# Optimization experiments

Hardware: AMD Instinct MI355X
Metric: run time of the kernel (lower is better)

Reference implementation:

```python
import jax, jax.numpy as jnp
import numpy as np

# conv_ada hyperparameters from init_kwargs: ka=1, alpha=0.25, kw=0.2
KA1 = 1.0          # activation scale for conv1 (ka)
KA2 = 1.25         # activation scale for conv2 (ka + alpha)
KW = 0.2           # weight clipping threshold used by the binary weight STE


def ste_sign(x, clip=1.0):
    """Binary sign with straight-through estimator (hardtanh-style clip).
    Forward value is sign(x); gradient is that of clip(x, -clip, clip)."""
    xc = jnp.clip(x, -clip, clip)
    return xc + jax.lax.stop_gradient(jnp.sign(x) - xc)


def conv_bin(x, w, ka, kw):
    """1-bit activation / 1-bit weight 3x3 conv (conv_ada).
    Activations -> ka * sign(x); weights -> per-out-channel mean(|w|) * sign(w)."""
    xq = ka * ste_sign(x)
    alpha_w = jnp.mean(jnp.abs(w), axis=(1, 2, 3), keepdims=True)  # [O,1,1,1]
    wq = alpha_w * ste_sign(w, kw)
    return jax.lax.conv_general_dilated(
        xq, wq, window_strides=(1, 1), padding='SAME',
        dimension_numbers=('NCHW', 'OIHW', 'NCHW'))


def prelu(x, slope):
    # per-channel PReLU, slope shape [C]
    return jnp.where(x >= 0, x, slope[None, :, None, None] * x)


def pixel_shuffle(x, r=2):
    b, c, h, w = x.shape
    co = c // (r * r)
    x = x.reshape(b, co, r, r, h, w)
    x = x.transpose(0, 1, 4, 2, 5, 3)  # b, co, h, r, w, r
    return x.reshape(b, co, h * r, w * r)


def setup_inputs() -> dict:
    key = jax.random.key(0)
    ks = jax.random.split(key, 11)
    B, C, H, W = 8, 64, 256, 256
    return {
        'x': jax.random.normal(ks[0], (B, C, H, W), jnp.float32),
        'w1': jax.random.normal(ks[1], (C, C, 3, 3), jnp.float32) * 0.1,
        'w2': jax.random.normal(ks[2], (2 * C, C, 3, 3), jnp.float32) * 0.1,
        'b_in': jax.random.normal(ks[3], (1, C, 1, 1), jnp.float32) * 0.01,
        'b1': jax.random.normal(ks[4], (1, C, 1, 1), jnp.float32) * 0.01,
        's1': jax.random.uniform(ks[5], (C,), jnp.float32) * 0.25,
        'b2': jax.random.normal(ks[6], (1, C, 1, 1), jnp.float32) * 0.01,
        'b2_': jax.random.normal(ks[7], (1, C, 1, 1), jnp.float32) * 0.01,
        'b3': jax.random.normal(ks[8], (1, 2 * C, 1, 1), jnp.float32) * 0.01,
        's2': jax.random.uniform(ks[9], (2 * C,), jnp.float32) * 0.25,
        'b4': jax.random.normal(ks[10], (1, 2 * C, 1, 1), jnp.float32) * 0.01,
    }


def reference(x, w1, w2, b_in, b1, s1, b2, b2_, b3, s2, b4):
    out = conv_bin(x + b_in, w1, KA1, KW)       # move1_ -> conv1
    xres = out + x                              # residual x = out + x
    # NOTE: in the original forward, move1 -> prelu1 -> move2 are computed on
    # `out` and then immediately overwritten by out = move2_(x); that branch
    # is dead code and does not affect the output (b1, s1, b2 get zero grads).
    out = conv_bin(xres + b2_, w2, KA2, KW)     # move2_ -> conv2
    out = out + jnp.concatenate([xres, xres], axis=1)  # shortcut = cat(x, x)
    out = prelu(out + b3, s2) + b4              # move3 -> prelu2 -> move4
    return pixel_shuffle(out, 2)                # [B, C/2, 2H, 2W]
```

## Files before the change

### kernel.cpp

```cpp
#include <hip/hip_runtime.h>
#include <hip/hip_bf16.h>

typedef unsigned long long u64;
typedef unsigned short ushort8 __attribute__((ext_vector_type(8)));

#define IMG_H 256
#define IMG_W 256
#define CIN   64
#define HW    (IMG_H * IMG_W)
#define NPIX  (8 * HW)

static __device__ __forceinline__ float bf16bits_to_f32(unsigned short h) {
    union { unsigned int u; float f; } c;
    c.u = ((unsigned int)h) << 16;
    return c.f;
}

__global__ void prep_kernel(const float* __restrict__ w1,
                            const float* __restrict__ w2,
                            u64* __restrict__ w1b, float* __restrict__ a1,
                            u64* __restrict__ w2b, float* __restrict__ a2) {
    int blk = blockIdx.x;
    int lane = threadIdx.x;
    const float* w;
    u64* wb;
    float* al;
    if (blk < 64) { w = w1 + (size_t)blk * 576;        wb = w1b + blk * 9;        al = a1 + blk; }
    else          { w = w2 + (size_t)(blk - 64) * 576; wb = w2b + (blk - 64) * 9; al = a2 + (blk - 64); }

    const float* wi = w + lane * 9;
    float s = 0.f;
    u64 bits[9];
#pragma unroll
    for (int t = 0; t < 9; ++t) {
        float v = wi[t];
        s += fabsf(v);
        bits[t] = __ballot(v > 0.f);
    }
#pragma unroll
    for (int m = 32; m >= 1; m >>= 1) s += __shfl_xor(s, m);
    if (lane == 0) {
        *al = s * (1.f / 576.f);
#pragma unroll
        for (int t = 0; t < 9; ++t) wb[t] = bits[t];
    }
}

__global__ __launch_bounds__(256)
void pack_kernel(const float* __restrict__ x,
                 const float* __restrict__ b_in,
                 u64* __restrict__ bits1) {
    int i = blockIdx.x * 256 + threadIdx.x;
    int n = i >> 16, p = i & 65535;
    const float* xp = x + (size_t)n * CIN * HW + p;
    u64 w = 0;
#pragma unroll
    for (int c = 0; c < 64; ++c)
        w |= (u64)((xp[(size_t)c * HW] + b_in[c]) > 0.f) << c;
    bits1[i] = w;
}

__global__ __launch_bounds__(256)
void conv1_kernel(const float* __restrict__ x,
                  const float* __restrict__ b2_,
                  const u64* __restrict__ bits1,
                  const u64* __restrict__ wbits,
                  const float* __restrict__ alpha1,
                  ushort8* __restrict__ xres,
                  u64* __restrict__ bits2) {
    int i = blockIdx.x * 256 + threadIdx.x;
    int n = i >> 16, p = i & 65535;
    int y = p >> 8, xc = p & 255;

    u64 xb[9];
    int invmask = 0, nv = 0;
#pragma unroll
    for (int t = 0; t < 9; ++t) {
        int dy = t / 3 - 1, dx = t % 3 - 1;
        bool v = ((unsigned)(y + dy) < (unsigned)IMG_H) &
                 ((unsigned)(xc + dx) < (unsigned)IMG_W);
        xb[t] = v ? bits1[i + dy * IMG_W + dx] : 0ull;
        invmask |= (v ? 0 : 1) << t;
        nv += v ? 1 : 0;
    }

    const float* xp = x + (size_t)n * CIN * HW + p;
    u64 w2 = 0;

#pragma unroll 1
    for (int g = 0; g < 8; ++g) {
        ushort8 pk;
#pragma unroll
        for (int j = 0; j < 8; ++j) {
            int o = g * 8 + j;
            const u64* wo = wbits + o * 9;
            int D = 0;
#pragma unroll
            for (int t = 0; t < 9; ++t) D += __popcll(xb[t] ^ wo[t]);
            int S = 64 * nv - 2 * D;
            if (invmask) {
                int Dc = 0;
#pragma unroll
                for (int t = 0; t < 9; ++t)
                    if ((invmask >> t) & 1) Dc += __popcll(wo[t]);
                S += 2 * Dc;
            }
            float r = alpha1[o] * (float)S + xp[(size_t)o * HW];
            __hip_bfloat16 hb = __float2bfloat16(r);
            pk[j] = *(unsigned short*)&hb;
            w2 |= (u64)((r + b2_[o]) > 0.f) << o;
        }
        xres[(size_t)(n * 8 + g) * HW + p] = pk;
    }
    bits2[i] = w2;
}

__global__ __launch_bounds__(256)
void conv2_kernel(const ushort8* __restrict__ xres,
                  const u64* __restrict__ bits2,
                  const u64* __restrict__ wbits,
                  const float* __restrict__ alpha2,
                  const float* __restrict__ b3,
                  const float* __restrict__ s2,
                  const float* __restrict__ b4,
                  float* __restrict__ out) {
    int i = blockIdx.x * 256 + threadIdx.x;
    int n = i >> 16, p = i & 65535;
    int y = p >> 8, xc = p & 255;

    u64 xb[9];
    int invmask = 0, nv = 0;
#pragma unroll
    for (int t = 0; t < 9; ++t) {
        int dy = t / 3 - 1, dx = t % 3 - 1;
        bool v = ((unsigned)(y + dy) < (unsigned)IMG_H) &
                 ((unsigned)(xc + dx) < (unsigned)IMG_W);
        xb[t] = v ? bits2[i + dy * IMG_W + dx] : 0ull;
        invmask |= (v ? 0 : 1) << t;
        nv += v ? 1 : 0;
    }

    float* ob = out + (size_t)n * 32 * 512 * 512;
    const int Y = 2 * y, X = 2 * xc;

#pragma unroll 1
    for (int g = 0; g < 8; ++g) {
        ushort8 xr = xres[(size_t)(n * 8 + g) * HW + p];
        float vlo[8], vhi[8];
#pragma unroll
        for (int j = 0; j < 8; ++j) {
            int o = g * 8 + j;
            float xrv = bf16bits_to_f32(xr[j]);
            {
                const u64* wo = wbits + o * 9;
                int D = 0;
#pragma unroll
                for (int t = 0; t < 9; ++t) D += __popcll(xb[t] ^ wo[t]);
                int S = 64 * nv - 2 * D;
                if (invmask) {
                    int Dc = 0;
#pragma unroll
                    for (int t = 0; t < 9; ++t)
                        if ((invmask >> t) & 1) Dc += __popcll(wo[t]);
                    S += 2 * Dc;
                }
                float u = 1.25f * alpha2[o] * (float)S + xrv + b3[o];
                u = (u >= 0.f) ? u : s2[o] * u;
                vlo[j] = u + b4[o];
            }
            {
                int o2 = o + 64;
                const u64* wo = wbits + o2 * 9;
                int D = 0;
#pragma unroll
                for (int t = 0; t < 9; ++t) D += __popcll(xb[t] ^ wo[t]);
                int S = 64 * nv - 2 * D;
                if (invmask) {
                    int Dc = 0;
#pragma unroll
                    for (int t = 0; t < 9; ++t)
                        if ((invmask >> t) & 1) Dc += __popcll(wo[t]);
                    S += 2 * Dc;
                }
                float u = 1.25f * alpha2[o2] * (float)S + xrv + b3[o2];
                u = (u >= 0.f) ? u : s2[o2] * u;
                vhi[j] = u + b4[o2];
            }
        }
#pragma unroll
        for (int jj = 0; jj < 8; jj += 2) {
            int o = g * 8 + jj;
            int co = o >> 2;
            int r1 = (o >> 1) & 1;
            *(float2*)(ob + ((size_t)co * 512 + Y + r1) * 512 + X) =
                make_float2(vlo[jj], vlo[jj + 1]);
            *(float2*)(ob + ((size_t)(co + 16) * 512 + Y + r1) * 512 + X) =
                make_float2(vhi[jj], vhi[jj + 1]);
        }
    }
}

extern "C" void kernel_launch(void* const* d_in, const int* in_sizes, int n_in,
                              void* d_out, int out_size, void* d_ws, size_t ws_size,
                              hipStream_t stream) {
    const float* x    = (const float*)d_in[0];
    const float* w1   = (const float*)d_in[1];
    const float* w2   = (const float*)d_in[2];
    const float* b_in = (const float*)d_in[3];
    const float* b2_  = (const float*)d_in[7];
    const float* b3   = (const float*)d_in[8];
    const float* s2   = (const float*)d_in[9];
    const float* b4   = (const float*)d_in[10];
    float* out = (float*)d_out;

    char* ws = (char*)d_ws;
    u64*   w1b   = (u64*)(ws + 0);
    u64*   w2b   = (u64*)(ws + 4608);
    float* a1    = (float*)(ws + 13824);
    float* a2    = (float*)(ws + 14080);
    u64*   bits1 = (u64*)(ws + 16384);
    u64*   bits2 = (u64*)(ws + 16384 + 4194304);
    ushort8* xres = (ushort8*)(ws + 16384 + 2 * 4194304);

    prep_kernel<<<192, 64, 0, stream>>>(w1, w2, w1b, a1, w2b, a2);

    const int nblk = NPIX / 256;
    pack_kernel <<<nblk, 256, 0, stream>>>(x, b_in, bits1);
    conv1_kernel<<<nblk, 256, 0, stream>>>(x, b2_, bits1, w1b, a1, xres, bits2);
    conv2_kernel<<<nblk, 256, 0, stream>>>(xres, bits2, w2b, a2, b3, s2, b4, out);
}
```

Measured before the change: 241.6 us.

## Vectorize pack loads, hoist conv1 residual loads, unroll loops, nontemporal output stores

The pack kernel now has each thread handle two pixels, using float2 loads and a 128-bit store of the packed bits, so it launches half as many blocks. conv1 loads the eight residual x values per group up front and builds the sign mask eight bits at a time. Both conv loops are unrolled by two, and conv2 writes its output with nontemporal stores to avoid polluting the cache. These changes aim to cut memory-instruction overhead and raise memory-level parallelism, at the cost of higher register pressure from unrolling.

```diff
diff --git a/kernel.cpp b/kernel.cpp
--- a/kernel.cpp
+++ b/kernel.cpp
@@ -2,7 +2,10 @@
 #include <hip/hip_bf16.h>
 
 typedef unsigned long long u64;
+typedef unsigned int u32;
 typedef unsigned short ushort8 __attribute__((ext_vector_type(8)));
+typedef u64 u64x2 __attribute__((ext_vector_type(2)));
+typedef float fx2 __attribute__((ext_vector_type(2)));
 
 #define IMG_H 256
 #define IMG_W 256
@@ -11,9 +14,13 @@
 #define NPIX  (8 * HW)
 
 static __device__ __forceinline__ float bf16bits_to_f32(unsigned short h) {
-    union { unsigned int u; float f; } c;
-    c.u = ((unsigned int)h) << 16;
+    union { u32 u; float f; } c;
+    c.u = ((u32)h) << 16;
     return c.f;
+}
+static __device__ __forceinline__ unsigned short f32_to_bf16bits(float f) {
+    __hip_bfloat16 hb = __float2bfloat16(f);
+    return *(unsigned short*)&hb;
 }
 
 __global__ void prep_kernel(const float* __restrict__ w1,
@@ -50,14 +57,29 @@
 void pack_kernel(const float* __restrict__ x,
                  const float* __restrict__ b_in,
                  u64* __restrict__ bits1) {
-    int i = blockIdx.x * 256 + threadIdx.x;
-    int n = i >> 16, p = i & 65535;
+    int tid = blockIdx.x * 256 + threadIdx.x;
+    int n = tid >> 15;
+    int p = (tid & 32767) * 2;
     const float* xp = x + (size_t)n * CIN * HW + p;
-    u64 w = 0;
-#pragma unroll
-    for (int c = 0; c < 64; ++c)
-        w |= (u64)((xp[(size_t)c * HW] + b_in[c]) > 0.f) << c;
-    bits1[i] = w;
+    u32 w0lo = 0, w0hi = 0, w1lo = 0, w1hi = 0;
+#pragma unroll
+    for (int c = 0; c < 32; ++c) {
+        fx2 v = *(const fx2*)(xp + (size_t)c * HW);
+        float b = b_in[c];
+        w0lo |= (u32)((v.x + b) > 0.f) << c;
+        w1lo |= (u32)((v.y + b) > 0.f) << c;
+    }
+#pragma unroll
+    for (int c = 0; c < 32; ++c) {
+        fx2 v = *(const fx2*)(xp + (size_t)(c + 32) * HW);
+        float b = b_in[c + 32];
+        w0hi |= (u32)((v.x + b) > 0.f) << c;
+        w1hi |= (u32)((v.y + b) > 0.f) << c;
+    }
+    u64x2 pk;
+    pk.x = ((u64)w0hi << 32) | w0lo;
+    pk.y = ((u64)w1hi << 32) | w1lo;
+    *(u64x2*)(bits1 + (size_t)n * HW + p) = pk;
 }
 
 __global__ __launch_bounds__(256)
@@ -87,9 +109,15 @@
     const float* xp = x + (size_t)n * CIN * HW + p;
     u64 w2 = 0;
 
-#pragma unroll 1
+#pragma unroll 2
     for (int g = 0; g < 8; ++g) {
+        float rv[8];
+#pragma unroll
+        for (int j = 0; j < 8; ++j)
+            rv[j] = xp[(size_t)(g * 8 + j) * HW];
+
         ushort8 pk;
+        u32 gm = 0;
 #pragma unroll
         for (int j = 0; j < 8; ++j) {
             int o = g * 8 + j;
@@ -99,18 +127,16 @@
             for (int t = 0; t < 9; ++t) D += __popcll(xb[t] ^ wo[t]);
             int S = 64 * nv - 2 * D;
             if (invmask) {
-                int Dc = 0;
 #pragma unroll
                 for (int t = 0; t < 9; ++t)
-                    if ((invmask >> t) & 1) Dc += __popcll(wo[t]);
-                S += 2 * Dc;
+                    if ((invmask >> t) & 1) S += 2 * __popcll(wo[t]);
             }
-            float r = alpha1[o] * (float)S + xp[(size_t)o * HW];
-            __hip_bfloat16 hb = __float2bfloat16(r);
-            pk[j] = *(unsigned short*)&hb;
-            w2 |= (u64)((r + b2_[o]) > 0.f) << o;
+            float r = alpha1[o] * (float)S + rv[j];
+            pk[j] = f32_to_bf16bits(r);
+            gm |= (u32)((r + b2_[o]) > 0.f) << j;
         }
         xres[(size_t)(n * 8 + g) * HW + p] = pk;
+        w2 |= (u64)gm << (8 * g);
     }
     bits2[i] = w2;
 }
@@ -143,7 +169,7 @@
     float* ob = out + (size_t)n * 32 * 512 * 512;
     const int Y = 2 * y, X = 2 * xc;
 
-#pragma unroll 1
+#pragma unroll 2
     for (int g = 0; g < 8; ++g) {
         ushort8 xr = xres[(size_t)(n * 8 + g) * HW + p];
         float vlo[8], vhi[8];
@@ -158,11 +184,9 @@
                 for (int t = 0; t < 9; ++t) D += __popcll(xb[t] ^ wo[t]);
                 int S = 64 * nv - 2 * D;
                 if (invmask) {
-                    int Dc = 0;
 #pragma unroll
                     for (int t = 0; t < 9; ++t)
-                        if ((invmask >> t) & 1) Dc += __popcll(wo[t]);
-                    S += 2 * Dc;
+                        if ((invmask >> t) & 1) S += 2 * __popcll(wo[t]);
                 }
                 float u = 1.25f * alpha2[o] * (float)S + xrv + b3[o];
                 u = (u >= 0.f) ? u : s2[o] * u;
@@ -176,11 +200,9 @@
                 for (int t = 0; t < 9; ++t) D += __popcll(xb[t] ^ wo[t]);
                 int S = 64 * nv - 2 * D;
                 if (invmask) {
-                    int Dc = 0;
 #pragma unroll
                     for (int t = 0; t < 9; ++t)
-                        if ((invmask >> t) & 1) Dc += __popcll(wo[t]);
-                    S += 2 * Dc;
+                        if ((invmask >> t) & 1) S += 2 * __popcll(wo[t]);
                 }
                 float u = 1.25f * alpha2[o2] * (float)S + xrv + b3[o2];
                 u = (u >= 0.f) ? u : s2[o2] * u;
@@ -192,10 +214,12 @@
             int o = g * 8 + jj;
             int co = o >> 2;
             int r1 = (o >> 1) & 1;
-            *(float2*)(ob + ((size_t)co * 512 + Y + r1) * 512 + X) =
-                make_float2(vlo[jj], vlo[jj + 1]);
-            *(float2*)(ob + ((size_t)(co + 16) * 512 + Y + r1) * 512 + X) =
-                make_float2(vhi[jj], vhi[jj + 1]);
+            fx2 vl; vl.x = vlo[jj]; vl.y = vlo[jj + 1];
+            fx2 vh; vh.x = vhi[jj]; vh.y = vhi[jj + 1];
+            __builtin_nontemporal_store(
+                vl, (fx2*)(ob + ((size_t)co * 512 + Y + r1) * 512 + X));
+            __builtin_nontemporal_store(
+                vh, (fx2*)(ob + ((size_t)(co + 16) * 512 + Y + r1) * 512 + X));
         }
     }
 }
@@ -224,8 +248,7 @@
 
     prep_kernel<<<192, 64, 0, stream>>>(w1, w2, w1b, a1, w2b, a2);
 
-    const int nblk = NPIX / 256;
-    pack_kernel <<<nblk, 256, 0, stream>>>(x, b_in, bits1);
-    conv1_kernel<<<nblk, 256, 0, stream>>>(x, b2_, bits1, w1b, a1, xres, bits2);
-    conv2_kernel<<<nblk, 256, 0, stream>>>(xres, bits2, w2b, a2, b3, s2, b4, out);
-}
+    pack_kernel <<<NPIX / 512, 256, 0, stream>>>(x, b_in, bits1);
+    conv1_kernel<<<NPIX / 256, 256, 0, stream>>>(x, b2_, bits1, w1b, a1, xres, bits2);
+    conv2_kernel<<<NPIX / 256, 256, 0, stream>>>(xres, bits2, w2b, a2, b3, s2, b4, out);
+}
```

New measurement: 218.7 us. 1.1x faster.
